# Optimization experiments

Hardware: AMD Instinct MI355X
Metric: run time of the kernel (lower is better)

The kernel has to match this reference:

```python
import jax, jax.numpy as jnp
import numpy as np

TIME_PERIOD = 0.5


def _splat_sum(inp, flow):
    """Summation forward-splatting (bilinear scatter-add).
    inp:  [B, C, H, W], flow: [B, 2, H, W] (flow[:,0]=dx, flow[:,1]=dy).
    """
    B, C, H, W = inp.shape
    ftype = inp.dtype
    # target (non-integer) coordinates for each source pixel
    fltX = flow[:, 0] + jnp.arange(W, dtype=ftype)[None, None, :]   # [B,H,W]
    fltY = flow[:, 1] + jnp.arange(H, dtype=ftype)[None, :, None]   # [B,H,W]
    x0f, y0f = jnp.floor(fltX), jnp.floor(fltY)
    x0, y0 = x0f.astype(jnp.int32), y0f.astype(jnp.int32)
    # 4 bilinear corners: NW, NE, SW, SE
    xi = jnp.stack([x0, x0 + 1, x0, x0 + 1])                        # [4,B,H,W]
    yi = jnp.stack([y0, y0, y0 + 1, y0 + 1])
    w = jnp.stack([
        (x0f + 1.0 - fltX) * (y0f + 1.0 - fltY),
        (fltX - x0f) * (y0f + 1.0 - fltY),
        (x0f + 1.0 - fltX) * (fltY - y0f),
        (fltX - x0f) * (fltY - y0f),
    ])                                                              # [4,B,H,W]
    valid = (xi >= 0) & (xi < W) & (yi >= 0) & (yi < H)
    N = H * W
    idx = jnp.where(valid, yi * W + xi, 0).reshape(4, B, N)
    idx = idx.transpose(1, 0, 2).reshape(B, 4 * N)                  # [B,4N]
    wv = jnp.where(valid, w, jnp.zeros((), ftype)).reshape(4, B, N)
    wv = wv.transpose(1, 0, 2)                                      # [B,4,N]
    contrib = (inp.reshape(B, C, 1, N) * wv[:, None]).reshape(B, C, 4 * N)

    def scatter_one(c, i):
        return jnp.zeros((C, N), ftype).at[:, i].add(c)

    out = jax.vmap(scatter_one)(contrib, idx)                       # [B,C,N]
    return out.reshape(B, C, H, W)


def softsplat_average(img, flow):
    """softsplat.FunctionSoftsplat(strType='average'): append ones channel,
    summation-splat, then divide by the splatted ones (0 -> 1)."""
    B, C, H, W = img.shape
    inp = jnp.concatenate([img, jnp.ones((B, 1, H, W), img.dtype)], axis=1)
    out = _splat_sum(inp, flow)
    norm = out[:, -1:]
    norm = jnp.where(norm == 0.0, jnp.ones((), img.dtype), norm)
    return out[:, :-1] / norm


def setup_inputs() -> dict:
    key = jax.random.key(0)
    k0, k1, kf = jax.random.split(key, 3)
    B, H, W = 2, 1080, 1920
    img0 = jax.random.normal(k0, (B, 3, H, W), dtype=jnp.float32)
    img1 = jax.random.normal(k1, (B, 3, H, W), dtype=jnp.float32)
    # scale flows to realistic multi-pixel displacements
    bi_flow = jax.random.normal(kf, (B, 4, H, W), dtype=jnp.float32) * 10.0
    return {"img0": img0, "img1": img1, "bi_flow": bi_flow}


def reference(img0, img1, bi_flow):
    flow_0t = bi_flow[:, :2] * TIME_PERIOD
    flow_1t = bi_flow[:, 2:4] * (1.0 - TIME_PERIOD)
    warped_img0 = softsplat_average(img0, flow_0t)
    warped_img1 = softsplat_average(img1, flow_1t)
    fused = jnp.concatenate([warped_img1 - warped_img0, img1 - img0], axis=1)
    return (fused, warped_img1, warped_img0)
```

## Files before the change

kernel.cpp:

```cpp
#include <hip/hip_runtime.h>
#include <hip/hip_fp16.h>

constexpr int B = 2;
constexpr int H = 1080;
constexpr int W = 1920;
constexpr int HW = H * W;
constexpr float SCALE = 1024.f;

constexpr int TW = 96, TH = 20;
constexpr int R  = 11;
constexpr int HALO_W = TW + 2 * R;
constexpr int HALO_H = TH + 2 * R;
constexpr int NCELL  = HALO_W * HALO_H;
constexpr int NTX = (W + TW - 1) / TW;
constexpr int NTY = (H + TH - 1) / TH;
constexpr int NTILES = NTX * NTY;

__device__ __forceinline__ void pkadd(__half2* p, float a, float b) {
    unsafeAtomicAdd(p, __float22half2_rn(make_float2(a, b)));
}

__global__ __launch_bounds__(256, 8) void splat_tiled(
    const float* __restrict__ img0,
    const float* __restrict__ img1,
    const float* __restrict__ flow,
    float* __restrict__ out)
{
    __shared__ __half2 sP[NCELL];

    int bid = blockIdx.x;
    int t   = bid % NTILES;
    int r   = bid / NTILES;
    int ph  = r & 1;
    int ib  = r >> 1;
    int b   = ib & 1;
    int i   = ib >> 1;
    int ty0 = (t / NTX) * TH;
    int tx0 = (t - (t / NTX) * NTX) * TW;
    int tid = threadIdx.x;

    const float* img = i ? img1 : img0;
    const float* flx = flow + ((size_t)b * 4 + (i ? 2 : 0)) * HW;
    const float* fly = flx + HW;
    const float* imgb = img + (size_t)b * 3 * HW;

    const float* pa = imgb + (size_t)(ph ? 2 : 0) * HW;
    const float* pb = imgb + (size_t)HW;
    __half2* gp = (__half2*)out + (size_t)(12 + (i * 2 + b) * 2 + ph) * HW;

    for (int c = tid; c < NCELL; c += 256) ((unsigned int*)sP)[c] = 0u;
    __syncthreads();

    constexpr int GPR = TW / 4;
    constexpr int NGRP = TW * TH / 4;
    for (int g = tid; g < NGRP; g += 256) {
        int row = g / GPR;
        int col = (g - row * GPR) * 4;
        int gy = ty0 + row;
        if (gy >= H) break;
        int gx0 = tx0 + col;
        int p = gy * W + gx0;
        float4 fx4 = *(const float4*)(flx + p);
        float4 fy4 = *(const float4*)(fly + p);
        float4 va4 = *(const float4*)(pa + p);
        float4 vb4;
        if (ph) { vb4 = make_float4(1.f, 1.f, 1.f, 1.f); }
        else    { vb4 = *(const float4*)(pb + p); }

#pragma unroll
        for (int j = 0; j < 4; ++j) {
            float fx = (&fx4.x)[j] * 0.5f;
            float fy = (&fy4.x)[j] * 0.5f;
            float va = (&va4.x)[j] * SCALE;
            float vb = (&vb4.x)[j] * SCALE;
            float fltX = (float)(gx0 + j) + fx;
            float fltY = (float)gy + fy;
            float x0f = floorf(fltX), y0f = floorf(fltY);
            int x0 = (int)x0f, y0 = (int)y0f;
            float ax = fltX - x0f, ay = fltY - y0f;
            float bx = 1.f - ax, by = 1.f - ay;
            int hx = x0 - (tx0 - R);
            int hy = y0 - (ty0 - R);
            float wgt[4] = { bx * by, ax * by, bx * ay, ax * ay };
#pragma unroll
            for (int k = 0; k < 4; ++k) {
                int dxk = k & 1, dyk = k >> 1;
                int hxx = hx + dxk, hyy = hy + dyk;
                float w = wgt[k];
                if ((unsigned)hxx < (unsigned)HALO_W && (unsigned)hyy < (unsigned)HALO_H) {
                    int cell = hyy * HALO_W + hxx;
                    pkadd(&sP[cell], va * w, vb * w);
                } else {
                    int xx = x0 + dxk, yy = y0 + dyk;
                    if ((unsigned)xx < (unsigned)W && (unsigned)yy < (unsigned)H) {
                        int gq = yy * W + xx;
                        pkadd(gp + gq, va * w, vb * w);
                    }
                }
            }
        }
    }
    __syncthreads();

    for (int c = tid; c < NCELL; c += 256) {
        unsigned int raw;
        __builtin_memcpy(&raw, &sP[c], 4);
        if (raw != 0u) {
            int hy = c / HALO_W;
            int hx = c - hy * HALO_W;
            int gx = tx0 - R + hx;
            int gy = ty0 - R + hy;
            if ((unsigned)gx < (unsigned)W && (unsigned)gy < (unsigned)H) {
                int gq = gy * W + gx;
                unsafeAtomicAdd(gp + gq, sP[c]);
            }
        }
    }
}

__device__ __forceinline__ float2 unpack_pair(float f) {
    __half2 h;
    __builtin_memcpy(&h, &f, sizeof(h));
    return __half22float2(h);
}

__global__ __launch_bounds__(256) void fuse_kernel(
    const float* __restrict__ img0,
    const float* __restrict__ img1,
    float* __restrict__ out)
{
    int t = blockIdx.x * blockDim.x + threadIdx.x;
    constexpr int NP4 = HW / 4;
    if (t >= NP4) return;

    float4* o4 = (float4*)out;

    float4 s[8];
#pragma unroll
    for (int k = 0; k < 8; ++k) s[k] = o4[(size_t)(12 + k) * NP4 + t];

#pragma unroll
    for (int b = 0; b < 2; ++b) {
        float4 W0[3], W1[3];
#pragma unroll
        for (int j = 0; j < 4; ++j) {
            float2 a0 = unpack_pair((&s[2 * b].x)[j]);
            float2 b0 = unpack_pair((&s[2 * b + 1].x)[j]);
            float2 a1 = unpack_pair((&s[4 + 2 * b].x)[j]);
            float2 b1 = unpack_pair((&s[5 + 2 * b].x)[j]);
            float inv0 = b0.y != 0.f ? 1.f / b0.y : 0.f;
            float inv1 = b1.y != 0.f ? 1.f / b1.y : 0.f;
            (&W0[0].x)[j] = a0.x * inv0;
            (&W0[1].x)[j] = a0.y * inv0;
            (&W0[2].x)[j] = b0.x * inv0;
            (&W1[0].x)[j] = a1.x * inv1;
            (&W1[1].x)[j] = a1.y * inv1;
            (&W1[2].x)[j] = b1.x * inv1;
        }
#pragma unroll
        for (int c = 0; c < 3; ++c) {
            size_t ip = (size_t)(b * 3 + c) * NP4 + t;
            float4 i0v = ((const float4*)img0)[ip];
            float4 i1v = ((const float4*)img1)[ip];
            o4[(size_t)(12 + b * 3 + c) * NP4 + t] = W1[c];
            o4[(size_t)(18 + b * 3 + c) * NP4 + t] = W0[c];
            float4 d, e;
            d.x = W1[c].x - W0[c].x; d.y = W1[c].y - W0[c].y;
            d.z = W1[c].z - W0[c].z; d.w = W1[c].w - W0[c].w;
            o4[(size_t)(b * 6 + c) * NP4 + t] = d;
            e.x = i1v.x - i0v.x; e.y = i1v.y - i0v.y;
            e.z = i1v.z - i0v.z; e.w = i1v.w - i0v.w;
            o4[(size_t)(b * 6 + 3 + c) * NP4 + t] = e;
        }
    }
}

extern "C" void kernel_launch(void* const* d_in, const int* in_sizes, int n_in,
                              void* d_out, int out_size, void* d_ws, size_t ws_size,
                              hipStream_t stream) {
    const float* img0 = (const float*)d_in[0];
    const float* img1 = (const float*)d_in[1];
    const float* flow = (const float*)d_in[2];
    float* out = (float*)d_out;
    (void)d_ws; (void)ws_size;

    hipMemsetAsync(out + 12 * (size_t)HW, 0, 8 * (size_t)HW * sizeof(float), stream);

    {
        int blocks = 2 * B * 2 * NTILES;
        splat_tiled<<<blocks, 256, 0, stream>>>(img0, img1, flow, out);
    }
    {
        int blocks = (HW / 4 + 255) / 256;
        fuse_kernel<<<blocks, 256, 0, stream>>>(img0, img1, out);
    }
}
```

Before: 644.5 us.

## Move img1-img0 difference into splat kernel and remap scratch planes

Computes the img1-img0 difference channels inside the splat kernel, in the blocks for image 1 phase 1, rather than in the fuse kernel. The fp16 accumulation planes are moved to slots chosen so the fuse kernel reads only its 4 packed planes per pixel without colliding with its own outputs, which lets fuse run one thread per batch-pixel for more parallelism. The row bound check is dropped because H divides evenly by the tile height. This cuts fuse-kernel traffic but adds extra streaming work to a subset of splat blocks and splits the memset into four calls.

Result: no change. 638.6 us (-0.9%).

```diff
diff --git a/kernel.cpp b/kernel.cpp
--- a/kernel.cpp
+++ b/kernel.cpp
@@ -46,7 +46,9 @@
 
     const float* pa = imgb + (size_t)(ph ? 2 : 0) * HW;
     const float* pb = imgb + (size_t)HW;
-    __half2* gp = (__half2*)out + (size_t)(12 + (i * 2 + b) * 2 + ph) * HW;
+    int pl = b ? (i ? (ph ? 15 : 8) : (ph ? 7 : 6))
+               : (i ? (ph ? 12 : 2) : (ph ? 1 : 0));
+    __half2* gp = (__half2*)out + (size_t)pl * HW;
 
     for (int c = tid; c < NCELL; c += 256) ((unsigned int*)sP)[c] = 0u;
     __syncthreads();
@@ -57,7 +59,6 @@
         int row = g / GPR;
         int col = (g - row * GPR) * 4;
         int gy = ty0 + row;
-        if (gy >= H) break;
         int gx0 = tx0 + col;
         int p = gy * W + gx0;
         float4 fx4 = *(const float4*)(flx + p);
@@ -116,6 +117,23 @@
             }
         }
     }
+
+    if (i == 1 && ph == 1) {
+        for (int g = tid; g < NGRP * 3; g += 256) {
+            int c  = g / NGRP;
+            int gg = g - c * NGRP;
+            int row = gg / GPR;
+            int col = (gg - row * GPR) * 4;
+            int p = (ty0 + row) * W + tx0 + col;
+            size_t o = ((size_t)b * 3 + c) * HW + p;
+            float4 i0v = *(const float4*)(img0 + o);
+            float4 i1v = *(const float4*)(img1 + o);
+            float4 e;
+            e.x = i1v.x - i0v.x; e.y = i1v.y - i0v.y;
+            e.z = i1v.z - i0v.z; e.w = i1v.w - i0v.w;
+            *(float4*)(out + ((size_t)b * 6 + 3 + c) * HW + p) = e;
+        }
+    }
 }
 
 __device__ __forceinline__ float2 unpack_pair(float f) {
@@ -124,54 +142,47 @@
     return __half22float2(h);
 }
 
-__global__ __launch_bounds__(256) void fuse_kernel(
-    const float* __restrict__ img0,
-    const float* __restrict__ img1,
-    float* __restrict__ out)
+__global__ __launch_bounds__(256) void fuse_kernel(float* __restrict__ out)
 {
     int t = blockIdx.x * blockDim.x + threadIdx.x;
     constexpr int NP4 = HW / 4;
-    if (t >= NP4) return;
+    if (t >= B * NP4) return;
+    int b  = t >= NP4;
+    int p4 = t - (b ? NP4 : 0);
 
     float4* o4 = (float4*)out;
-
-    float4 s[8];
-#pragma unroll
-    for (int k = 0; k < 8; ++k) s[k] = o4[(size_t)(12 + k) * NP4 + t];
-
-#pragma unroll
-    for (int b = 0; b < 2; ++b) {
-        float4 W0[3], W1[3];
-#pragma unroll
-        for (int j = 0; j < 4; ++j) {
-            float2 a0 = unpack_pair((&s[2 * b].x)[j]);
-            float2 b0 = unpack_pair((&s[2 * b + 1].x)[j]);
-            float2 a1 = unpack_pair((&s[4 + 2 * b].x)[j]);
-            float2 b1 = unpack_pair((&s[5 + 2 * b].x)[j]);
-            float inv0 = b0.y != 0.f ? 1.f / b0.y : 0.f;
-            float inv1 = b1.y != 0.f ? 1.f / b1.y : 0.f;
-            (&W0[0].x)[j] = a0.x * inv0;
-            (&W0[1].x)[j] = a0.y * inv0;
-            (&W0[2].x)[j] = b0.x * inv0;
-            (&W1[0].x)[j] = a1.x * inv1;
-            (&W1[1].x)[j] = a1.y * inv1;
-            (&W1[2].x)[j] = b1.x * inv1;
-        }
-#pragma unroll
-        for (int c = 0; c < 3; ++c) {
-            size_t ip = (size_t)(b * 3 + c) * NP4 + t;
-            float4 i0v = ((const float4*)img0)[ip];
-            float4 i1v = ((const float4*)img1)[ip];
-            o4[(size_t)(12 + b * 3 + c) * NP4 + t] = W1[c];
-            o4[(size_t)(18 + b * 3 + c) * NP4 + t] = W0[c];
-            float4 d, e;
-            d.x = W1[c].x - W0[c].x; d.y = W1[c].y - W0[c].y;
-            d.z = W1[c].z - W0[c].z; d.w = W1[c].w - W0[c].w;
-            o4[(size_t)(b * 6 + c) * NP4 + t] = d;
-            e.x = i1v.x - i0v.x; e.y = i1v.y - i0v.y;
-            e.z = i1v.z - i0v.z; e.w = i1v.w - i0v.w;
-            o4[(size_t)(b * 6 + 3 + c) * NP4 + t] = e;
-        }
+    const int pa0 = b ? 6 : 0, pb0 = b ? 7 : 1;
+    const int pa1 = b ? 8 : 2, pb1 = b ? 15 : 12;
+
+    float4 s0a = o4[(size_t)pa0 * NP4 + p4];
+    float4 s0b = o4[(size_t)pb0 * NP4 + p4];
+    float4 s1a = o4[(size_t)pa1 * NP4 + p4];
+    float4 s1b = o4[(size_t)pb1 * NP4 + p4];
+
+    float4 W0[3], W1[3];
+#pragma unroll
+    for (int j = 0; j < 4; ++j) {
+        float2 a0 = unpack_pair((&s0a.x)[j]);
+        float2 b0 = unpack_pair((&s0b.x)[j]);
+        float2 a1 = unpack_pair((&s1a.x)[j]);
+        float2 b1 = unpack_pair((&s1b.x)[j]);
+        float inv0 = b0.y != 0.f ? 1.f / b0.y : 0.f;
+        float inv1 = b1.y != 0.f ? 1.f / b1.y : 0.f;
+        (&W0[0].x)[j] = a0.x * inv0;
+        (&W0[1].x)[j] = a0.y * inv0;
+        (&W0[2].x)[j] = b0.x * inv0;
+        (&W1[0].x)[j] = a1.x * inv1;
+        (&W1[1].x)[j] = a1.y * inv1;
+        (&W1[2].x)[j] = b1.x * inv1;
+    }
+#pragma unroll
+    for (int c = 0; c < 3; ++c) {
+        float4 d;
+        d.x = W1[c].x - W0[c].x; d.y = W1[c].y - W0[c].y;
+        d.z = W1[c].z - W0[c].z; d.w = W1[c].w - W0[c].w;
+        o4[((size_t)b * 6 + c) * NP4 + p4]      = d;
+        o4[(size_t)(12 + b * 3 + c) * NP4 + p4] = W1[c];
+        o4[(size_t)(18 + b * 3 + c) * NP4 + p4] = W0[c];
     }
 }
 
@@ -184,14 +195,17 @@
     float* out = (float*)d_out;
     (void)d_ws; (void)ws_size;
 
-    hipMemsetAsync(out + 12 * (size_t)HW, 0, 8 * (size_t)HW * sizeof(float), stream);
+    hipMemsetAsync(out,                  0, 3 * (size_t)HW * sizeof(float), stream);
+    hipMemsetAsync(out +  6 * (size_t)HW, 0, 3 * (size_t)HW * sizeof(float), stream);
+    hipMemsetAsync(out + 12 * (size_t)HW, 0, (size_t)HW * sizeof(float), stream);
+    hipMemsetAsync(out + 15 * (size_t)HW, 0, (size_t)HW * sizeof(float), stream);
 
     {
         int blocks = 2 * B * 2 * NTILES;
         splat_tiled<<<blocks, 256, 0, stream>>>(img0, img1, flow, out);
     }
     {
-        int blocks = (HW / 4 + 255) / 256;
-        fuse_kernel<<<blocks, 256, 0, stream>>>(img0, img1, out);
-    }
-}
+        int blocks = (B * (HW / 4) + 255) / 256;
+        fuse_kernel<<<blocks, 256, 0, stream>>>(out);
+    }
+}
```
